# Performance work log

Measured on AMD Instinct MI355X. Metric: run time of the kernel, lower is better.

The kernel has to match this reference:

```python
import jax, jax.numpy as jnp
import numpy as np

WS = (2, 7, 7)   # window size (D,H,W)
SS = (1, 3, 3)   # shift size
NUM_HEADS = 12
EPS = 1e-5


def _window_partition(x, ws):
    B, D, H, W, C = x.shape
    x = x.reshape(B, D // ws[0], ws[0], H // ws[1], ws[1], W // ws[2], ws[2], C)
    return x.transpose(0, 1, 3, 5, 2, 4, 6, 7).reshape(-1, ws[0] * ws[1] * ws[2], C)


def _window_reverse(win, ws, B, D, H, W):
    x = win.reshape(B, D // ws[0], H // ws[1], W // ws[2], ws[0], ws[1], ws[2], -1)
    return x.transpose(0, 1, 4, 2, 5, 3, 6, 7).reshape(B, D, H, W, -1)


def _relative_position_index(ws):
    coords = np.stack(np.meshgrid(np.arange(ws[0]), np.arange(ws[1]), np.arange(ws[2]), indexing='ij'))
    cf = coords.reshape(3, -1)
    rel = (cf[:, :, None] - cf[:, None, :]).transpose(1, 2, 0)
    rel[:, :, 0] += ws[0] - 1
    rel[:, :, 1] += ws[1] - 1
    rel[:, :, 2] += ws[2] - 1
    rel[:, :, 0] *= (2 * ws[1] - 1) * (2 * ws[2] - 1)
    rel[:, :, 1] *= 2 * ws[2] - 1
    return rel.sum(-1)  # (N, N)


def _compute_mask(D, H, W, ws, ss):
    img = np.zeros((1, D, H, W, 1), dtype=np.float32)
    def sl(w, s):
        return [slice(-w), slice(-w, -s), slice(-s, None)] if s > 0 else [slice(None)]
    cnt = 0
    for d in sl(ws[0], ss[0]):
        for h in sl(ws[1], ss[1]):
            for w in sl(ws[2], ss[2]):
                img[:, d, h, w, :] = cnt
                cnt += 1
    # numpy window partition
    x = img.reshape(1, D // ws[0], ws[0], H // ws[1], ws[1], W // ws[2], ws[2], 1)
    mw = x.transpose(0, 1, 3, 5, 2, 4, 6, 7).reshape(-1, ws[0] * ws[1] * ws[2])
    diff = mw[:, None, :] - mw[:, :, None]
    return np.where(diff != 0, -100.0, 0.0).astype(np.float32)  # (nW, N, N)


def _layernorm(x, w, b):
    m = x.mean(-1, keepdims=True)
    v = ((x - m) ** 2).mean(-1, keepdims=True)
    return (x - m) * jax.lax.rsqrt(v + EPS) * w + b


def setup_inputs() -> dict:
    key = jax.random.key(0)
    ks = jax.random.split(key, 16)
    C = 384
    Hd = 4 * C
    nB = (2 * WS[0] - 1) * (2 * WS[1] - 1) * (2 * WS[2] - 1)
    s = lambda k, shape, f=0.02: jax.random.normal(k, shape, jnp.float32) * f
    return {
        'x': jax.random.normal(ks[0], (2, 8, 56, 56, C), jnp.float32),
        'norm1_w': jnp.ones((C,), jnp.float32), 'norm1_b': jnp.zeros((C,), jnp.float32),
        'qkv_w': s(ks[1], (3 * C, C)), 'qkv_b': jnp.zeros((3 * C,), jnp.float32),
        'rpb_table': s(ks[2], (nB, NUM_HEADS)),
        'proj_w': s(ks[3], (C, C)), 'proj_b': jnp.zeros((C,), jnp.float32),
        'norm2_w': jnp.ones((C,), jnp.float32), 'norm2_b': jnp.zeros((C,), jnp.float32),
        'fc1_w': s(ks[4], (Hd, C)), 'fc1_b': jnp.zeros((Hd,), jnp.float32),
        'fc2_w': s(ks[5], (C, Hd)), 'fc2_b': jnp.zeros((C,), jnp.float32),
    }


def reference(x, norm1_w, norm1_b, qkv_w, qkv_b, rpb_table, proj_w, proj_b,
              norm2_w, norm2_b, fc1_w, fc1_b, fc2_w, fc2_b):
    B, D, H, W, C = x.shape
    h = NUM_HEADS
    hd = C // h
    scale = hd ** -0.5
    N = WS[0] * WS[1] * WS[2]

    shortcut = x
    xn = _layernorm(x, norm1_w, norm1_b)
    # dims are exact multiples of window size -> no padding needed
    shifted = jnp.roll(xn, shift=(-SS[0], -SS[1], -SS[2]), axis=(1, 2, 3))
    xw = _window_partition(shifted, WS)  # (B_, N, C)
    B_ = xw.shape[0]

    qkv = (xw @ qkv_w.T + qkv_b).reshape(B_, N, 3, h, hd).transpose(2, 0, 3, 1, 4)
    q, k, v = qkv[0], qkv[1], qkv[2]  # (B_, h, N, hd)
    attn = jnp.einsum('bhnd,bhmd->bhnm', q * scale, k)

    rel_idx = _relative_position_index(WS)  # static numpy (N, N)
    bias = rpb_table[rel_idx.reshape(-1)].reshape(N, N, h).transpose(2, 0, 1)
    attn = attn + bias[None]

    mask = jnp.asarray(_compute_mask(D, H, W, WS, SS))  # (nW, N, N)
    nW = mask.shape[0]
    attn = attn.reshape(B_ // nW, nW, h, N, N) + mask[None, :, None]
    attn = jax.nn.softmax(attn.reshape(B_, h, N, N), axis=-1)

    out = jnp.einsum('bhnm,bhmd->bhnd', attn, v).transpose(0, 2, 1, 3).reshape(B_, N, C)
    out = out @ proj_w.T + proj_b

    xr = _window_reverse(out, WS, B, D, H, W)
    xr = jnp.roll(xr, shift=SS, axis=(1, 2, 3))
    x = shortcut + xr  # drop_path = 0

    y = _layernorm(x, norm2_w, norm2_b)
    y = jax.nn.gelu(y @ fc1_w.T + fc1_b, approximate=False) @ fc2_w.T + fc2_b
    return x + y
```

## Files before the change

kernel.cpp:

```cpp
#include <hip/hip_runtime.h>
#include <hip/hip_bf16.h>

typedef __hip_bfloat16 bf16;
typedef __attribute__((ext_vector_type(8))) short bf16x8;
typedef __attribute__((ext_vector_type(4))) float f32x4;

__device__ __forceinline__ float tof(bf16 v) { return __bfloat162float(v); }
__device__ __forceinline__ float ldf(const float* p) { return *p; }
__device__ __forceinline__ float ldf(const bf16* p) { return __bfloat162float(*p); }
__device__ __forceinline__ void stf(float* p, float v) { *p = v; }
__device__ __forceinline__ void stf(bf16* p, float v) { *p = __float2bfloat16(v); }
__device__ __forceinline__ short bfbits(float v) {
    return (short)__builtin_bit_cast(unsigned short, __float2bfloat16(v));
}

__device__ __forceinline__ void gl2lds16(const void* g, void* l) {
    __builtin_amdgcn_global_load_lds((const __attribute__((address_space(1))) void*)g,
                                     (__attribute__((address_space(3))) void*)l, 16, 0, 0);
}

constexpr int TOK   = 50176;
constexpr int CCH   = 384;
constexpr int NELEM = TOK * CCH;
constexpr int BT_N  = 8 * 12 * 98 * 112;

__device__ __forceinline__ int remap_row(int m) {
    int b_ = m / 98, n = m % 98;
    int b = b_ >> 8, wrem = b_ & 255;
    int dw = wrem >> 6, hw = (wrem >> 3) & 7, wwi = wrem & 7;
    int zd = n / 49, r = n % 49, zh = r / 7, zw = r % 7;
    int d = ((dw * 2 + zd) + 1) & 7;
    int h = hw * 7 + zh + 3; if (h >= 56) h -= 56;
    int w = wwi * 7 + zw + 3; if (w >= 56) w -= 56;
    return ((b * 8 + d) * 56 + h) * 56 + w;
}

template <bool SRC_INPUT>
__global__ __launch_bounds__(256) void ln_kernel(const void* __restrict__ srcv,
                                                 const float* __restrict__ g,
                                                 const float* __restrict__ be,
                                                 bf16* __restrict__ dst) {
    int wave = threadIdx.x >> 6, lane = threadIdx.x & 63;
    int t = blockIdx.x * 4 + wave;
    int srcRow = SRC_INPUT ? remap_row(t) : t;
    float v[6];
    float s = 0.f, ss = 0.f;
#pragma unroll
    for (int j = 0; j < 6; ++j) {
        size_t idx = (size_t)srcRow * CCH + lane + 64 * j;
        v[j] = SRC_INPUT ? ((const float*)srcv)[idx] : tof(((const bf16*)srcv)[idx]);
        s += v[j];
        ss += v[j] * v[j];
    }
#pragma unroll
    for (int off = 32; off; off >>= 1) {
        s  += __shfl_xor(s, off, 64);
        ss += __shfl_xor(ss, off, 64);
    }
    float mean = s * (1.f / 384.f);
    float var  = ss * (1.f / 384.f) - mean * mean;
    float rstd = rsqrtf(var + 1e-5f);
    bf16* q = dst + (size_t)t * CCH;
#pragma unroll
    for (int j = 0; j < 6; ++j) {
        int c = lane + 64 * j;
        stf(q + c, (v[j] - mean) * rstd * g[c] + be[c]);
    }
}

__global__ __launch_bounds__(256) void cvt_split(const float* __restrict__ w,
                                                 bf16* __restrict__ hi,
                                                 bf16* __restrict__ lo, int n) {
    int i = blockIdx.x * 256 + threadIdx.x;
    if (i >= n) return;
    float f = w[i];
    bf16 h = __float2bfloat16(f);
    hi[i] = h;
    lo[i] = __float2bfloat16(f - __bfloat162float(h));
}

__global__ __launch_bounds__(256) void bias_precomp(const float* __restrict__ rpb,
                                                    float* __restrict__ table) {
    int bid = blockIdx.x;
    int cls = bid / 12, head = bid % 12;
    int cd = (cls >> 2) & 1, ch = (cls >> 1) & 1, cw = cls & 1;
    for (int e = threadIdx.x; e < 98 * 112; e += 256) {
        int i = e / 112, j = e % 112;
        float v;
        if (j >= 98) {
            v = -1e30f;
        } else {
            int di = i / 49, ri = i % 49, hi = ri / 7, wi = ri % 7;
            int dj = j / 49, rj = j % 49, hj = rj / 7, wj = rj % 7;
            int idx = (di - dj + 1) * 169 + (hi - hj + 6) * 13 + (wi - wj + 6);
            v = rpb[(size_t)idx * 12 + head];
            int ci = (cd ? (1 + di) : 0) * 9 + (ch ? (hi < 4 ? 1 : 2) : 0) * 3 +
                     (cw ? (wi < 4 ? 1 : 2) : 0);
            int cj = (cd ? (1 + dj) : 0) * 9 + (ch ? (hj < 4 ? 1 : 2) : 0) * 3 +
                     (cw ? (wj < 4 ? 1 : 2) : 0);
            if (ci != cj) v -= 100.f;
        }
        table[(size_t)bid * 98 * 112 + e] = v;
    }
}

template <int MODE, typename CT, typename XT>
__global__ __launch_bounds__(256, 2) void gemm_mfma(const bf16* __restrict__ A, int lda,
                                                    const bf16* __restrict__ Bh,
                                                    const bf16* __restrict__ Bl, int ldb,
                                                    const float* __restrict__ bias,
                                                    CT* __restrict__ Cc, int ldc,
                                                    const XT* __restrict__ Xres,
                                                    int M, int K) {
    __shared__ short As[2][4096];
    __shared__ short Bhs[2][4096];
    __shared__ short Bls[2][4096];
    const int tid  = threadIdx.x;
    const int lane = tid & 63;
    const int wv   = tid >> 6;
    const int wm   = wv >> 1, wn = wv & 1;
    const int nwg  = gridDim.x * gridDim.y;
    const int orig = blockIdx.y * gridDim.x + blockIdx.x;
    const int q8 = nwg >> 3, r8 = nwg & 7;
    const int xcd = orig & 7, slot = orig >> 3;
    const int work = (xcd < r8) ? xcd * (q8 + 1) + slot
                                : r8 * (q8 + 1) + (xcd - r8) * q8 + slot;
    const int bm = (work / gridDim.x) * 128, bn = (work % gridDim.x) * 128;
    const int kb = lane >> 4, r15 = lane & 15;

    f32x4 acc[4][4] = {};

    const int i0   = tid, i1 = 256 + tid;
    const int kbb0 = i0 >> 7, kbb1 = i1 >> 7;
    const int row0 = (i0 & 127) ^ (kbb0 << 1);
    const int row1 = (i1 & 127) ^ (kbb1 << 1);
    int mrow0 = bm + row0; if (mrow0 >= M) mrow0 = M - 1;
    int mrow1 = bm + row1; if (mrow1 >= M) mrow1 = M - 1;
    const int ls0 = (0 * 256 + (wv << 6)) * 8;
    const int ls1 = (1 * 256 + (wv << 6)) * 8;

#define STAGE(buf, k0)                                                              \
    do {                                                                            \
        gl2lds16(A  + (size_t)mrow0 * lda + (k0) + kbb0 * 8, &As[buf][ls0]);        \
        gl2lds16(Bh + (size_t)(bn + row0) * ldb + (k0) + kbb0 * 8, &Bhs[buf][ls0]); \
        gl2lds16(Bl + (size_t)(bn + row0) * ldb + (k0) + kbb0 * 8, &Bls[buf][ls0]); \
        gl2lds16(A  + (size_t)mrow1 * lda + (k0) + kbb1 * 8, &As[buf][ls1]);        \
        gl2lds16(Bh + (size_t)(bn + row1) * ldb + (k0) + kbb1 * 8, &Bhs[buf][ls1]); \
        gl2lds16(Bl + (size_t)(bn + row1) * ldb + (k0) + kbb1 * 8, &Bls[buf][ls1]); \
    } while (0)

    STAGE(0, 0);
    __syncthreads();

    const int nk = K >> 5;
    int cur = 0;
    for (int t = 0; t < nk; ++t) {
        if (t + 1 < nk) STAGE(cur ^ 1, (t + 1) * 32);

        bf16x8 af[4];
#pragma unroll
        for (int im = 0; im < 4; ++im) {
            const int row = wm * 64 + im * 16 + r15;
            af[im] = *(const bf16x8*)&As[cur][(kb * 128 + (row ^ (kb << 1))) * 8];
        }
#pragma unroll
        for (int in = 0; in < 4; ++in) {
            const int col = wn * 64 + in * 16 + r15;
            const int sl  = (kb * 128 + (col ^ (kb << 1))) * 8;
            const bf16x8 bh = *(const bf16x8*)&Bhs[cur][sl];
            const bf16x8 bl = *(const bf16x8*)&Bls[cur][sl];
#pragma unroll
            for (int im = 0; im < 4; ++im) {
                acc[im][in] = __builtin_amdgcn_mfma_f32_16x16x32_bf16(af[im], bh, acc[im][in], 0, 0, 0);
                acc[im][in] = __builtin_amdgcn_mfma_f32_16x16x32_bf16(af[im], bl, acc[im][in], 0, 0, 0);
            }
        }
        __syncthreads();
        cur ^= 1;
    }
#undef STAGE

#pragma unroll
    for (int im = 0; im < 4; ++im) {
        const int mb = bm + wm * 64 + im * 16 + (lane >> 4) * 4;
#pragma unroll
        for (int in = 0; in < 4; ++in) {
            const int c = bn + wn * 64 + in * 16 + r15;
            const float bv = bias[c];
#pragma unroll
            for (int r = 0; r < 4; ++r) {
                const int m = mb + r;
                if (m >= M) continue;
                float v = acc[im][in][r] + bv;
                if (MODE == 0) {
                    stf(Cc + (size_t)m * ldc + c, v);
                } else if (MODE == 1) {
                    size_t xi = (size_t)remap_row(m) * ldc + c;
                    stf(Cc + xi, ldf(Xres + xi) + v);
                } else if (MODE == 2) {
                    float u  = v * fmaf(0.0356774081f, v * v, 0.7978845608f);
                    float e  = __expf(2.f * u);
                    float th = 1.f - 2.f * __builtin_amdgcn_rcpf(e + 1.f);
                    stf(Cc + (size_t)m * ldc + c, 0.5f * v * (1.f + th));
                } else {
                    size_t xi = (size_t)m * ldc + c;
                    stf(Cc + xi, ldf(Xres + xi) + v);
                }
            }
        }
    }
}

__global__ __launch_bounds__(64) void attn_kernel(const bf16* __restrict__ qkv,
                                                  const float* __restrict__ bt,
                                                  bf16* __restrict__ outw, int gbase) {
    __shared__ short Vs[112 * 32];
    __shared__ short Ps[16 * 128];
    const int bid  = blockIdx.x;
    const int head = bid % 12;
    const int brel = bid / 12;
    const int babs = gbase + brel;
    const int lane = threadIdx.x;
    const int g = lane >> 4, c15 = lane & 15;

    const size_t qbase = (size_t)brel * 98 * 1152 + head * 32;

#pragma unroll
    for (int it = 0; it < 7; ++it) {
        int c = it * 64 + lane;
        int j = c >> 2, e0 = (c & 3) * 8;
        int jc = j < 98 ? j : 97;
        *(bf16x8*)&Vs[j * 32 + e0] =
            *(const bf16x8*)(qkv + qbase + (size_t)jc * 1152 + 768 + e0);
    }
    if (lane < 32) {
        int i = lane >> 1, half = lane & 1;
        int pb = (14 + half) ^ (i & 7);
        *(bf16x8*)&Ps[i * 128 + pb * 8] = bf16x8{0, 0, 0, 0, 0, 0, 0, 0};
    }

    bf16x8 qf[7], kf[7];
#pragma unroll
    for (int t7 = 0; t7 < 7; ++t7) {
        int qi = t7 * 16 + c15; if (qi > 97) qi = 97;
        const bf16* rp = qkv + qbase + (size_t)qi * 1152 + g * 8;
        qf[t7] = *(const bf16x8*)rp;
        kf[t7] = *(const bf16x8*)(rp + 384);
    }
    __syncthreads();

    bf16x8 vb[4][2];
#pragma unroll
    for (int kb = 0; kb < 4; ++kb)
#pragma unroll
        for (int t = 0; t < 2; ++t) {
            bf16x8 f;
#pragma unroll
            for (int e = 0; e < 8; ++e) {
                int j = kb * 32 + g * 8 + e;
                int jv = j < 112 ? j : 111;
                f[e] = Vs[jv * 32 + t * 16 + c15];
            }
            vb[kb][t] = f;
        }

    const int cls = ((((babs >> 6) & 3) == 3) ? 4 : 0) |
                    ((((babs >> 3) & 7) == 7) ? 2 : 0) |
                    (((babs & 7) == 7) ? 1 : 0);
    const float* btb = bt + (size_t)(cls * 12 + head) * 98 * 112;
    const float scale = 0.17677669529663687f;

#pragma unroll 1
    for (int it = 0; it < 7; ++it) {
        f32x4 s[7];
#pragma unroll
        for (int jt = 0; jt < 7; ++jt)
            s[jt] = __builtin_amdgcn_mfma_f32_16x16x32_bf16(qf[it], kf[jt],
                                                            f32x4{0, 0, 0, 0}, 0, 0, 0);
#pragma unroll
        for (int jt = 0; jt < 7; ++jt)
#pragma unroll
            for (int r = 0; r < 4; ++r) {
                int i = it * 16 + g * 4 + r; if (i > 97) i = 97;
                s[jt][r] = fmaf(s[jt][r], scale, btb[i * 112 + jt * 16 + c15]);
            }
        float mx[4], inv[4];
#pragma unroll
        for (int r = 0; r < 4; ++r) {
            float m = s[0][r];
#pragma unroll
            for (int jt = 1; jt < 7; ++jt) m = fmaxf(m, s[jt][r]);
#pragma unroll
            for (int off = 8; off; off >>= 1) m = fmaxf(m, __shfl_xor(m, off, 64));
            mx[r] = m;
        }
#pragma unroll
        for (int jt = 0; jt < 7; ++jt)
#pragma unroll
            for (int r = 0; r < 4; ++r) s[jt][r] = __expf(s[jt][r] - mx[r]);
#pragma unroll
        for (int r = 0; r < 4; ++r) {
            float t = 0.f;
#pragma unroll
            for (int jt = 0; jt < 7; ++jt) t += s[jt][r];
#pragma unroll
            for (int off = 8; off; off >>= 1) t += __shfl_xor(t, off, 64);
            inv[r] = 1.f / t;
        }
#pragma unroll
        for (int jt = 0; jt < 7; ++jt)
#pragma unroll
            for (int r = 0; r < 4; ++r) {
                int i = g * 4 + r;
                int j = jt * 16 + c15;
                int pj = ((((j >> 3) ^ (i & 7)) << 3)) | (j & 7);
                Ps[i * 128 + pj] = bfbits(s[jt][r]);
            }
        f32x4 o[2] = {f32x4{0, 0, 0, 0}, f32x4{0, 0, 0, 0}};
#pragma unroll
        for (int kb = 0; kb < 4; ++kb) {
            int pb = (kb * 4 + g) ^ (c15 & 7);
            bf16x8 pa = *(const bf16x8*)&Ps[c15 * 128 + pb * 8];
#pragma unroll
            for (int t = 0; t < 2; ++t)
                o[t] = __builtin_amdgcn_mfma_f32_16x16x32_bf16(pa, vb[kb][t], o[t], 0, 0, 0);
        }
#pragma unroll
        for (int t = 0; t < 2; ++t)
#pragma unroll
            for (int r = 0; r < 4; ++r) {
                int i = it * 16 + g * 4 + r;
                if (i < 98)
                    stf(outw + ((size_t)babs * 98 + i) * 384 + head * 32 + t * 16 + c15,
                        o[t][r] * inv[r]);
            }
    }
}

extern "C" void kernel_launch(void* const* d_in, const int* in_sizes, int n_in,
                              void* d_out, int out_size, void* d_ws, size_t ws_size,
                              hipStream_t stream) {
    const float* x      = (const float*)d_in[0];
    const float* n1w    = (const float*)d_in[1];
    const float* n1b    = (const float*)d_in[2];
    const float* qkv_w  = (const float*)d_in[3];
    const float* qkv_b  = (const float*)d_in[4];
    const float* rpb    = (const float*)d_in[5];
    const float* proj_w = (const float*)d_in[6];
    const float* proj_b = (const float*)d_in[7];
    const float* n2w    = (const float*)d_in[8];
    const float* n2b    = (const float*)d_in[9];
    const float* fc1_w  = (const float*)d_in[10];
    const float* fc1_b  = (const float*)d_in[11];
    const float* fc2_w  = (const float*)d_in[12];
    const float* fc2_b  = (const float*)d_in[13];

    bf16*  aout = (bf16*)d_out;
    float* btab = (float*)((char*)d_out + (size_t)NELEM * 2);
    bf16*  xn2  = (bf16*)((char*)d_out + (size_t)NELEM * 2);
    float* fout = (float*)d_out;

    constexpr int QKV_WN  = 1152 * 384;
    constexpr int PROJ_WN = 384 * 384;
    constexpr int FC1_WN  = 1536 * 384;
    constexpr int FC2_WN  = 384 * 1536;
    bf16* qh   = (bf16*)d_ws;
    bf16* ql   = qh  + QKV_WN;
    bf16* ph   = ql  + QKV_WN;
    bf16* pl   = ph  + PROJ_WN;
    bf16* f1h  = pl  + PROJ_WN;
    bf16* f1l  = f1h + FC1_WN;
    bf16* f2h  = f1l + FC1_WN;
    bf16* f2l  = f2h + FC2_WN;
    bf16* rA   = f2l + FC2_WN;
    bf16* rC   = rA + (size_t)NELEM;
    size_t used    = (size_t)((char*)rC - (char*)d_ws);
    size_t rCbytes = (ws_size > used) ? ws_size - used : 0;

    cvt_split<<<(QKV_WN  + 255) / 256, 256, 0, stream>>>(qkv_w,  qh,  ql,  QKV_WN);
    cvt_split<<<(PROJ_WN + 255) / 256, 256, 0, stream>>>(proj_w, ph,  pl,  PROJ_WN);
    cvt_split<<<(FC1_WN  + 255) / 256, 256, 0, stream>>>(fc1_w,  f1h, f1l, FC1_WN);
    cvt_split<<<(FC2_WN  + 255) / 256, 256, 0, stream>>>(fc2_w,  f2h, f2l, FC2_WN);
    bias_precomp<<<96, 256, 0, stream>>>(rpb, btab);

    int W = 512;
    while (W > 1 && (size_t)W * 98 * 1152 * 2 > rCbytes) W >>= 1;
    int nqg = 512 / W;
    int ngm = 1;
    while (ngm < 1024 && (size_t)(TOK / ngm) * 1536 * 2 > rCbytes) ngm <<= 1;
    int Mt = TOK / ngm;

    dim3 blk(256);

    ln_kernel<true><<<dim3(TOK / 4), blk, 0, stream>>>(x, n1w, n1b, rA);
    for (int g = 0; g < nqg; ++g) {
        int Mg = W * 98;
        gemm_mfma<0, bf16, float><<<dim3(1152 / 128, (Mg + 127) / 128), blk, 0, stream>>>(
            rA + (size_t)g * Mg * 384, 384, qh, ql, 384, qkv_b,
            rC, 1152, (const float*)nullptr, Mg, 384);
        attn_kernel<<<dim3(W * 12), dim3(64), 0, stream>>>(rC, btab, aout, g * W);
    }
    gemm_mfma<1, bf16, float><<<dim3(384 / 128, TOK / 128), blk, 0, stream>>>(
        aout, 384, ph, pl, 384, proj_b, rA, 384, x, TOK, 384);
    ln_kernel<false><<<dim3(TOK / 4), blk, 0, stream>>>(rA, n2w, n2b, xn2);
    for (int g = 0; g < ngm; ++g) {
        size_t off = (size_t)g * Mt * 384;
        gemm_mfma<2, bf16, float><<<dim3(1536 / 128, (Mt + 127) / 128), blk, 0, stream>>>(
            xn2 + off, 384, f1h, f1l, 384, fc1_b, rC, 1536, (const float*)nullptr, Mt, 384);
        gemm_mfma<4, float, bf16><<<dim3(384 / 128, (Mt + 127) / 128), blk, 0, stream>>>(
            rC, 1536, f2h, f2l, 1536, fc2_b, fout + off, 384, rA + off, Mt, 1536);
    }
}
```

Baseline: 1.173 ms.

## Triple-buffer GEMM LDS staging with explicit vmcnt waits and barriers

Moves the MFMA GEMM from double to triple buffering in LDS, prefetching three K-slices ahead with async global-to-LDS loads. Blocking __syncthreads is replaced by counted s_waitcnt vmcnt waits and raw s_barrier, so up to two stages of loads stay in flight while the current stage is computed. The aim is to hide global memory latency better. In exchange LDS use rises from 48 KB to 72 KB per block, which may reduce occupancy at launch_bounds(256,2), and the hand-counted vmcnt values must match the six loads per stage exactly.

```diff
diff --git a/kernel.cpp b/kernel.cpp
--- a/kernel.cpp
+++ b/kernel.cpp
@@ -112,9 +112,9 @@
                                                     CT* __restrict__ Cc, int ldc,
                                                     const XT* __restrict__ Xres,
                                                     int M, int K) {
-    __shared__ short As[2][4096];
-    __shared__ short Bhs[2][4096];
-    __shared__ short Bls[2][4096];
+    __shared__ short As[3][4096];
+    __shared__ short Bhs[3][4096];
+    __shared__ short Bls[3][4096];
     const int tid  = threadIdx.x;
     const int lane = tid & 63;
     const int wv   = tid >> 6;
@@ -136,26 +136,30 @@
     const int row1 = (i1 & 127) ^ (kbb1 << 1);
     int mrow0 = bm + row0; if (mrow0 >= M) mrow0 = M - 1;
     int mrow1 = bm + row1; if (mrow1 >= M) mrow1 = M - 1;
-    const int ls0 = (0 * 256 + (wv << 6)) * 8;
-    const int ls1 = (1 * 256 + (wv << 6)) * 8;
-
-#define STAGE(buf, k0)                                                              \
-    do {                                                                            \
-        gl2lds16(A  + (size_t)mrow0 * lda + (k0) + kbb0 * 8, &As[buf][ls0]);        \
-        gl2lds16(Bh + (size_t)(bn + row0) * ldb + (k0) + kbb0 * 8, &Bhs[buf][ls0]); \
-        gl2lds16(Bl + (size_t)(bn + row0) * ldb + (k0) + kbb0 * 8, &Bls[buf][ls0]); \
-        gl2lds16(A  + (size_t)mrow1 * lda + (k0) + kbb1 * 8, &As[buf][ls1]);        \
-        gl2lds16(Bh + (size_t)(bn + row1) * ldb + (k0) + kbb1 * 8, &Bhs[buf][ls1]); \
-        gl2lds16(Bl + (size_t)(bn + row1) * ldb + (k0) + kbb1 * 8, &Bls[buf][ls1]); \
+    const int ls0 = ((wv << 6)) * 8;
+    const int ls1 = (256 + (wv << 6)) * 8;
+
+#define STAGE(buf, k0)                                                                   \
+    do {                                                                                 \
+        gl2lds16(A  + (size_t)mrow0 * lda + (k0) + kbb0 * 8, &As[buf][ls0]);             \
+        gl2lds16(Bh + (size_t)(bn + row0) * ldb + (k0) + kbb0 * 8, &Bhs[buf][ls0]);      \
+        gl2lds16(Bl + (size_t)(bn + row0) * ldb + (k0) + kbb0 * 8, &Bls[buf][ls0]);      \
+        gl2lds16(A  + (size_t)mrow1 * lda + (k0) + kbb1 * 8, &As[buf][ls1]);             \
+        gl2lds16(Bh + (size_t)(bn + row1) * ldb + (k0) + kbb1 * 8, &Bhs[buf][ls1]);      \
+        gl2lds16(Bl + (size_t)(bn + row1) * ldb + (k0) + kbb1 * 8, &Bls[buf][ls1]);      \
     } while (0)
 
+    const int nk = K >> 5;
+
     STAGE(0, 0);
-    __syncthreads();
-
-    const int nk = K >> 5;
-    int cur = 0;
+    STAGE(1, 32);
+    STAGE(2, 64);
+    asm volatile("s_waitcnt vmcnt(12)" ::: "memory");
+    __builtin_amdgcn_sched_barrier(0);
+    __builtin_amdgcn_s_barrier();
+
     for (int t = 0; t < nk; ++t) {
-        if (t + 1 < nk) STAGE(cur ^ 1, (t + 1) * 32);
+        const int cur = t % 3;
 
         bf16x8 af[4];
 #pragma unroll
@@ -175,8 +179,22 @@
                 acc[im][in] = __builtin_amdgcn_mfma_f32_16x16x32_bf16(af[im], bl, acc[im][in], 0, 0, 0);
             }
         }
-        __syncthreads();
-        cur ^= 1;
+
+        if (t + 3 < nk) {
+            __builtin_amdgcn_s_barrier();
+            STAGE(cur, (t + 3) * 32);
+        }
+        if (t + 1 < nk) {
+            if (t + 3 < nk) {
+                asm volatile("s_waitcnt vmcnt(12)" ::: "memory");
+            } else if (t + 2 < nk) {
+                asm volatile("s_waitcnt vmcnt(6)" ::: "memory");
+            } else {
+                asm volatile("s_waitcnt vmcnt(0)" ::: "memory");
+            }
+            __builtin_amdgcn_sched_barrier(0);
+            __builtin_amdgcn_s_barrier();
+        }
     }
 #undef STAGE
 
```

Measured after the change: 1.339 ms. 14.1% more time.
